# Optimization experiments

Hardware: AMD Instinct MI355X
Metric: run time of the kernel (lower is better)

Reference implementation:

```python
import jax, jax.numpy as jnp
import numpy as np

B, I, O, K = 4096, 1024, 1024, 16

def setup_inputs() -> dict:
    key = jax.random.key(0)
    k1, k2 = jax.random.split(key)
    x = jax.random.normal(k1, (B, I), dtype=jnp.float32)
    weights = jax.random.normal(k2, (O, I, K), dtype=jnp.float32)
    bias = jnp.zeros((O,), dtype=jnp.float32)
    centers = jnp.linspace(-1.0, 1.0, K, dtype=jnp.float32)
    widths = jnp.full((K,), 0.1, dtype=jnp.float32)
    return {"x": x, "weights": weights, "bias": bias, "centers": centers, "widths": widths}

def reference(x, weights, bias, centers, widths):
    # Gaussian RBF basis: [B, I, K]
    diff = x[:, :, None] - centers[None, None, :]
    kernels = jnp.exp(-(diff ** 2) / (2.0 * widths[None, None, :] ** 2))
    # Contraction over input_dim and num_kernels (GEMM-equivalent)
    out = jnp.einsum('bik,oik->bo', kernels, weights)
    return out + bias
```

## Files before the change

### kernel.cpp

```cpp
#include <hip/hip_runtime.h>
#include <hip/hip_bf16.h>


#define B_DIM 4096
#define I_DIM 1024
#define O_DIM 1024
#define NK 16
#define KD (I_DIM * NK)

typedef unsigned short u16;
typedef __attribute__((ext_vector_type(8))) __bf16 bf16x8;
typedef __attribute__((ext_vector_type(4))) float f32x4;
typedef __attribute__((ext_vector_type(8))) unsigned short u16x8;

typedef const __attribute__((address_space(1))) unsigned short gu16;
typedef __attribute__((address_space(3))) unsigned short lu16;

static __device__ __forceinline__ u16 f2bf(float f) {
  unsigned u = __float_as_uint(f);
  u += 0x7FFFu + ((u >> 16) & 1u);
  return (u16)(u >> 16);
}

__global__ void __launch_bounds__(256) rbf_feat(const float* __restrict__ x,
                                                u16* __restrict__ feat,
                                                const float* __restrict__ centers,
                                                const float* __restrict__ widths) {
  const int idx = blockIdx.x * 256 + threadIdx.x;
  const float xv = x[idx];
  u16x8 lo, hi;
#pragma unroll
  for (int k = 0; k < 16; ++k) {
    const float c = centers[k];
    const float w = widths[k];
    const float s = -0.5f * __builtin_amdgcn_rcpf(w * w);
    const float d = xv - c;
    const u16 h = f2bf(__expf(d * d * s));
    if (k < 8) lo[k] = h; else hi[k - 8] = h;
  }
  u16x8* dst = (u16x8*)(feat + (size_t)idx * 16);
  dst[0] = lo;
  dst[1] = hi;
}

__global__ void __launch_bounds__(256) cvt_w(const float4* __restrict__ w,
                                             u16x8* __restrict__ wb) {
  const size_t i = (size_t)blockIdx.x * 256 + threadIdx.x;
  const float4 a = w[2 * i];
  const float4 b = w[2 * i + 1];
  u16x8 o;
  o[0] = f2bf(a.x); o[1] = f2bf(a.y); o[2] = f2bf(a.z); o[3] = f2bf(a.w);
  o[4] = f2bf(b.x); o[5] = f2bf(b.y); o[6] = f2bf(b.z); o[7] = f2bf(b.w);
  wb[i] = o;
}

static __device__ __forceinline__ void stage_half(const u16* __restrict__ g,
                                                  u16* __restrict__ lds, int t) {
#pragma unroll
  for (int j = 0; j < 2; ++j) {
    const int chunk = j * 512 + t;
    const int row = chunk >> 3, slot = chunk & 7;
    const int c = slot ^ (row & 7);
    __builtin_amdgcn_global_load_lds((gu16*)(g + (size_t)row * KD + c * 8),
                                     (lu16*)(lds + chunk * 8), 16, 0, 0);
  }
}

#define NT 64

__global__ void __launch_bounds__(512, 2)
gemm8(const u16* __restrict__ A, const u16* __restrict__ Bm,
      float* __restrict__ part) {
  __shared__ u16 sA[2][2][128 * 64];
  __shared__ u16 sB[2][2][128 * 64];

  const int t = threadIdx.x;
  const int bm = blockIdx.x;
  const int bn = blockIdx.y;
  const int kz = blockIdx.z;
  const int wid = t >> 6, l = t & 63;
  const int wr = wid >> 2, wc = wid & 3;
  const int lm = l & 15, lk = l >> 4;

  const u16* aT = A + (size_t)(bm * 256) * KD + kz * 4096;
  const u16* bT = Bm + (size_t)(bn * 256) * KD + kz * 4096;

  const int swz0 = ((0 * 4 + lk) ^ (lm & 7)) * 8;
  const int swz1 = ((1 * 4 + lk) ^ (lm & 7)) * 8;
  const int arow = wr * 64 + lm;
  const int brow = wc * 32 + lm;

  f32x4 acc[8][4];
#pragma unroll
  for (int i = 0; i < 8; ++i)
#pragma unroll
    for (int j = 0; j < 4; ++j)
      acc[i][j] = (f32x4){0.f, 0.f, 0.f, 0.f};

  stage_half(aT, &sA[0][0][0], t);
  stage_half(aT + (size_t)128 * KD, &sA[0][1][0], t);
  stage_half(bT, &sB[0][0][0], t);
  stage_half(bT + (size_t)128 * KD, &sB[0][1][0], t);
  asm volatile("s_waitcnt vmcnt(0)" ::: "memory");
  __builtin_amdgcn_s_barrier();

  for (int T = 0; T < NT; ++T) {
    const int c = T & 1;

    if (T + 1 < NT) {
      const int kn = (T + 1) * 64;
      stage_half(aT + kn, &sA[c ^ 1][0][0], t);
      stage_half(aT + (size_t)128 * KD + kn, &sA[c ^ 1][1][0], t);
      stage_half(bT + kn, &sB[c ^ 1][0][0], t);
      stage_half(bT + (size_t)128 * KD + kn, &sB[c ^ 1][1][0], t);
    }

    bf16x8 aq[4][2], aq2[4][2], b0[2][2], b1[2][2];
#pragma unroll
    for (int mi = 0; mi < 4; ++mi) {
      aq[mi][0]  = *(const bf16x8*)&sA[c][0][(arow + mi * 16) * 64 + swz0];
      aq[mi][1]  = *(const bf16x8*)&sA[c][0][(arow + mi * 16) * 64 + swz1];
      aq2[mi][0] = *(const bf16x8*)&sA[c][1][(arow + mi * 16) * 64 + swz0];
      aq2[mi][1] = *(const bf16x8*)&sA[c][1][(arow + mi * 16) * 64 + swz1];
    }
#pragma unroll
    for (int ni = 0; ni < 2; ++ni) {
      b0[ni][0] = *(const bf16x8*)&sB[c][0][(brow + ni * 16) * 64 + swz0];
      b0[ni][1] = *(const bf16x8*)&sB[c][0][(brow + ni * 16) * 64 + swz1];
      b1[ni][0] = *(const bf16x8*)&sB[c][1][(brow + ni * 16) * 64 + swz0];
      b1[ni][1] = *(const bf16x8*)&sB[c][1][(brow + ni * 16) * 64 + swz1];
    }

    __builtin_amdgcn_s_setprio(1);
#pragma unroll
    for (int mi = 0; mi < 4; ++mi)
#pragma unroll
      for (int ni = 0; ni < 2; ++ni)
#pragma unroll
        for (int kk = 0; kk < 2; ++kk)
          acc[mi][ni] = __builtin_amdgcn_mfma_f32_16x16x32_bf16(
              aq[mi][kk], b0[ni][kk], acc[mi][ni], 0, 0, 0);
#pragma unroll
    for (int mi = 0; mi < 4; ++mi)
#pragma unroll
      for (int ni = 0; ni < 2; ++ni)
#pragma unroll
        for (int kk = 0; kk < 2; ++kk)
          acc[mi][2 + ni] = __builtin_amdgcn_mfma_f32_16x16x32_bf16(
              aq[mi][kk], b1[ni][kk], acc[mi][2 + ni], 0, 0, 0);
#pragma unroll
    for (int mi = 0; mi < 4; ++mi)
#pragma unroll
      for (int ni = 0; ni < 2; ++ni)
#pragma unroll
        for (int kk = 0; kk < 2; ++kk)
          acc[4 + mi][2 + ni] = __builtin_amdgcn_mfma_f32_16x16x32_bf16(
              aq2[mi][kk], b1[ni][kk], acc[4 + mi][2 + ni], 0, 0, 0);
#pragma unroll
    for (int mi = 0; mi < 4; ++mi)
#pragma unroll
      for (int ni = 0; ni < 2; ++ni)
#pragma unroll
        for (int kk = 0; kk < 2; ++kk)
          acc[4 + mi][ni] = __builtin_amdgcn_mfma_f32_16x16x32_bf16(
              aq2[mi][kk], b0[ni][kk], acc[4 + mi][ni], 0, 0, 0);
    __builtin_amdgcn_s_setprio(0);

    asm volatile("s_waitcnt vmcnt(0)" ::: "memory");
    __builtin_amdgcn_s_barrier();
  }

  float* pW = part + (size_t)kz * ((size_t)B_DIM * O_DIM);
#pragma unroll
  for (int qa = 0; qa < 2; ++qa)
#pragma unroll
    for (int mi = 0; mi < 4; ++mi)
#pragma unroll
      for (int qb = 0; qb < 2; ++qb)
#pragma unroll
        for (int ni = 0; ni < 2; ++ni) {
          const int row0 = bm * 256 + qa * 128 + wr * 64 + mi * 16 + lk * 4;
          const int col = bn * 256 + qb * 128 + wc * 32 + ni * 16 + lm;
#pragma unroll
          for (int j = 0; j < 4; ++j)
            pW[(size_t)(row0 + j) * O_DIM + col] = acc[qa * 4 + mi][qb * 2 + ni][j];
        }
}

__global__ void __launch_bounds__(256) reduce4(const float4* __restrict__ p,
                                               const float4* __restrict__ bias4,
                                               float4* __restrict__ out) {
  const int i = blockIdx.x * 256 + threadIdx.x;
  const size_t s = (size_t)B_DIM * O_DIM / 4;
  const float4 a = p[i], b = p[i + s], c = p[i + 2 * s], d = p[i + 3 * s];
  const float4 bb = bias4[i & 255];
  float4 r;
  r.x = a.x + b.x + c.x + d.x + bb.x;
  r.y = a.y + b.y + c.y + d.y + bb.y;
  r.z = a.z + b.z + c.z + d.z + bb.z;
  r.w = a.w + b.w + c.w + d.w + bb.w;
  out[i] = r;
}

#define BM 128
#define BN 64
#define BK 64

__global__ void __launch_bounds__(256, 2) gemm_bt(const u16* __restrict__ A,
                                                  const u16* __restrict__ Bm,
                                                  const float* __restrict__ bias,
                                                  float* __restrict__ C) {
  __shared__ u16 sA[BM * BK];
  __shared__ u16 sB[BN * BK];

  const int t = threadIdx.x;
  const int bm = blockIdx.x, bn = blockIdx.y;
  const int wid = t >> 6, l = t & 63;
  const int wr = wid >> 1, wc = wid & 1;
  const int lm = l & 15, lk = l >> 4;

  const u16* aG = A + (size_t)bm * BM * KD;
  const u16* bG = Bm + (size_t)bn * BN * KD;

  f32x4 acc[4][2];
#pragma unroll
  for (int mi = 0; mi < 4; ++mi)
#pragma unroll
    for (int ni = 0; ni < 2; ++ni)
      acc[mi][ni] = (f32x4){0.f, 0.f, 0.f, 0.f};

  for (int kt = 0; kt < KD; kt += BK) {
#pragma unroll
    for (int j = 0; j < 4; ++j) {
      const int chunk = j * 256 + t;
      const int row = chunk >> 3, slot = chunk & 7;
      const int c = slot ^ (row & 7);
      __builtin_amdgcn_global_load_lds((gu16*)(aG + (size_t)row * KD + kt + c * 8),
                                       (lu16*)(sA + chunk * 8), 16, 0, 0);
    }
#pragma unroll
    for (int j = 0; j < 2; ++j) {
      const int chunk = j * 256 + t;
      const int row = chunk >> 3, slot = chunk & 7;
      const int c = slot ^ (row & 7);
      __builtin_amdgcn_global_load_lds((gu16*)(bG + (size_t)row * KD + kt + c * 8),
                                       (lu16*)(sB + chunk * 8), 16, 0, 0);
    }
    __syncthreads();
#pragma unroll
    for (int kk = 0; kk < 2; ++kk) {
      const int s = (kk * 4 + lk) ^ (lm & 7);
      bf16x8 af[4], bfr[2];
#pragma unroll
      for (int mi = 0; mi < 4; ++mi)
        af[mi] = *(const bf16x8*)(sA + (wr * 64 + mi * 16 + lm) * BK + s * 8);
#pragma unroll
      for (int ni = 0; ni < 2; ++ni)
        bfr[ni] = *(const bf16x8*)(sB + (wc * 32 + ni * 16 + lm) * BK + s * 8);
#pragma unroll
      for (int mi = 0; mi < 4; ++mi)
#pragma unroll
        for (int ni = 0; ni < 2; ++ni)
          acc[mi][ni] = __builtin_amdgcn_mfma_f32_16x16x32_bf16(af[mi], bfr[ni],
                                                                acc[mi][ni], 0, 0, 0);
    }
    __syncthreads();
  }

#pragma unroll
  for (int ni = 0; ni < 2; ++ni) {
    const int col = bn * BN + wc * 32 + ni * 16 + lm;
    const float bv = bias[col];
#pragma unroll
    for (int mi = 0; mi < 4; ++mi) {
      const int row0 = bm * BM + wr * 64 + mi * 16 + lk * 4;
#pragma unroll
      for (int j = 0; j < 4; ++j)
        C[(size_t)(row0 + j) * O_DIM + col] = acc[mi][ni][j] + bv;
    }
  }
}

extern "C" void kernel_launch(void* const* d_in, const int* in_sizes, int n_in,
                              void* d_out, int out_size, void* d_ws, size_t ws_size,
                              hipStream_t stream) {
  const float* x = (const float*)d_in[0];
  const float* w = (const float*)d_in[1];
  const float* bias = (const float*)d_in[2];
  const float* centers = (const float*)d_in[3];
  const float* widths = (const float*)d_in[4];
  float* out = (float*)d_out;

  u16* feat = (u16*)d_ws;
  u16* wb = (u16*)((char*)d_ws + (size_t)B_DIM * KD * 2);
  float* part = (float*)((char*)d_ws + (size_t)B_DIM * KD * 2 + (size_t)O_DIM * KD * 2);

  rbf_feat<<<(B_DIM * I_DIM) / 256, 256, 0, stream>>>(x, feat, centers, widths);
  cvt_w<<<(O_DIM * KD) / (256 * 8), 256, 0, stream>>>((const float4*)w, (u16x8*)wb);

  const size_t need = (size_t)B_DIM * KD * 2 + (size_t)O_DIM * KD * 2 +
                      4ull * B_DIM * O_DIM * 4;
  if (ws_size >= need) {
    dim3 grid(B_DIM / 256, O_DIM / 256, 4);
    gemm8<<<grid, 512, 0, stream>>>(feat, wb, part);
    reduce4<<<(B_DIM * O_DIM / 4) / 256, 256, 0, stream>>>(
        (const float4*)part, (const float4*)bias, (float4*)out);
  } else {
    dim3 grid(B_DIM / BM, O_DIM / BN);
    gemm_bt<<<grid, 256, 0, stream>>>(feat, wb, bias, out);
  }
}
```

Before: 197.3 us.

## Prefetch first K-half tiles two stages ahead with triple-buffered LDS

Splits the A/B shared buffers into per-half arrays, triple-buffering the first 128-row halves and double-buffering the second halves. First halves are loaded two iterations ahead while second halves stay one ahead, and the end-of-iteration wait is relaxed to vmcnt(4) so the newest loads stay in flight across the barrier. This aims to hide more global-to-LDS latency behind MFMA work, at the cost of raising LDS use to the full 160KB and adding more complex indexing.

Result: no change. 198.6 us (+0.6%).

```diff
diff --git a/kernel.cpp b/kernel.cpp
--- a/kernel.cpp
+++ b/kernel.cpp
@@ -71,8 +71,10 @@
 __global__ void __launch_bounds__(512, 2)
 gemm8(const u16* __restrict__ A, const u16* __restrict__ Bm,
       float* __restrict__ part) {
-  __shared__ u16 sA[2][2][128 * 64];
-  __shared__ u16 sB[2][2][128 * 64];
+  __shared__ u16 sA0[3][128 * 64];
+  __shared__ u16 sB0[3][128 * 64];
+  __shared__ u16 sA1[2][128 * 64];
+  __shared__ u16 sB1[2][128 * 64];
 
   const int t = threadIdx.x;
   const int bm = blockIdx.x;
@@ -97,38 +99,44 @@
     for (int j = 0; j < 4; ++j)
       acc[i][j] = (f32x4){0.f, 0.f, 0.f, 0.f};
 
-  stage_half(aT, &sA[0][0][0], t);
-  stage_half(aT + (size_t)128 * KD, &sA[0][1][0], t);
-  stage_half(bT, &sB[0][0][0], t);
-  stage_half(bT + (size_t)128 * KD, &sB[0][1][0], t);
-  asm volatile("s_waitcnt vmcnt(0)" ::: "memory");
+  stage_half(aT, &sA0[0][0], t);
+  stage_half(aT + (size_t)128 * KD, &sA1[0][0], t);
+  stage_half(bT, &sB0[0][0], t);
+  stage_half(bT + (size_t)128 * KD, &sB1[0][0], t);
+  stage_half(bT + 64, &sB0[1][0], t);
+  stage_half(aT + 64, &sA0[1][0], t);
+  asm volatile("s_waitcnt vmcnt(4)" ::: "memory");
   __builtin_amdgcn_s_barrier();
 
   for (int T = 0; T < NT; ++T) {
-    const int c = T & 1;
+    const int c3 = T % 3;
+    const int c2 = T & 1;
 
     if (T + 1 < NT) {
-      const int kn = (T + 1) * 64;
-      stage_half(aT + kn, &sA[c ^ 1][0][0], t);
-      stage_half(aT + (size_t)128 * KD + kn, &sA[c ^ 1][1][0], t);
-      stage_half(bT + kn, &sB[c ^ 1][0][0], t);
-      stage_half(bT + (size_t)128 * KD + kn, &sB[c ^ 1][1][0], t);
+      const int kn1 = (T + 1) * 64;
+      stage_half(aT + (size_t)128 * KD + kn1, &sA1[(T + 1) & 1][0], t);
+      stage_half(bT + (size_t)128 * KD + kn1, &sB1[(T + 1) & 1][0], t);
+    }
+    if (T + 2 < NT) {
+      const int kn2 = (T + 2) * 64;
+      stage_half(bT + kn2, &sB0[(T + 2) % 3][0], t);
+      stage_half(aT + kn2, &sA0[(T + 2) % 3][0], t);
     }
 
     bf16x8 aq[4][2], aq2[4][2], b0[2][2], b1[2][2];
 #pragma unroll
     for (int mi = 0; mi < 4; ++mi) {
-      aq[mi][0]  = *(const bf16x8*)&sA[c][0][(arow + mi * 16) * 64 + swz0];
-      aq[mi][1]  = *(const bf16x8*)&sA[c][0][(arow + mi * 16) * 64 + swz1];
-      aq2[mi][0] = *(const bf16x8*)&sA[c][1][(arow + mi * 16) * 64 + swz0];
-      aq2[mi][1] = *(const bf16x8*)&sA[c][1][(arow + mi * 16) * 64 + swz1];
+      aq[mi][0]  = *(const bf16x8*)&sA0[c3][(arow + mi * 16) * 64 + swz0];
+      aq[mi][1]  = *(const bf16x8*)&sA0[c3][(arow + mi * 16) * 64 + swz1];
+      aq2[mi][0] = *(const bf16x8*)&sA1[c2][(arow + mi * 16) * 64 + swz0];
+      aq2[mi][1] = *(const bf16x8*)&sA1[c2][(arow + mi * 16) * 64 + swz1];
     }
 #pragma unroll
     for (int ni = 0; ni < 2; ++ni) {
-      b0[ni][0] = *(const bf16x8*)&sB[c][0][(brow + ni * 16) * 64 + swz0];
-      b0[ni][1] = *(const bf16x8*)&sB[c][0][(brow + ni * 16) * 64 + swz1];
-      b1[ni][0] = *(const bf16x8*)&sB[c][1][(brow + ni * 16) * 64 + swz0];
-      b1[ni][1] = *(const bf16x8*)&sB[c][1][(brow + ni * 16) * 64 + swz1];
+      b0[ni][0] = *(const bf16x8*)&sB0[c3][(brow + ni * 16) * 64 + swz0];
+      b0[ni][1] = *(const bf16x8*)&sB0[c3][(brow + ni * 16) * 64 + swz1];
+      b1[ni][0] = *(const bf16x8*)&sB1[c2][(brow + ni * 16) * 64 + swz0];
+      b1[ni][1] = *(const bf16x8*)&sB1[c2][(brow + ni * 16) * 64 + swz1];
     }
 
     __builtin_amdgcn_s_setprio(1);
@@ -166,7 +174,8 @@
               aq2[mi][kk], b0[ni][kk], acc[4 + mi][ni], 0, 0, 0);
     __builtin_amdgcn_s_setprio(0);
 
-    asm volatile("s_waitcnt vmcnt(0)" ::: "memory");
+    if (T + 2 < NT) asm volatile("s_waitcnt vmcnt(4)" ::: "memory");
+    else            asm volatile("s_waitcnt vmcnt(0)" ::: "memory");
     __builtin_amdgcn_s_barrier();
   }
 
```

## Shrink split-K GEMM tile to 128x128 with 256 threads and remapped block order

Applied to the files above, without the earlier changes.

Replaces the 256x256 tile, 512-thread split-K GEMM with a 128x128 tile, 256-thread kernel. Each wave keeps a 64x64 output subtile, and blocks are launched four times as many (1024 total). Block IDs are remapped so consecutive blocks spread across XCD-like groups of 8 and share A/B panels in cache. The aim is better load balance and occupancy across CUs. In exchange, the smaller tiles reuse operands less and generate more global/LDS traffic per FLOP.

Result: slower. 286.7 us (+45.3%).

```diff
diff --git a/kernel.cpp b/kernel.cpp
--- a/kernel.cpp
+++ b/kernel.cpp
@@ -54,11 +54,11 @@
   wb[i] = o;
 }
 
-static __device__ __forceinline__ void stage_half(const u16* __restrict__ g,
+static __device__ __forceinline__ void stage_tile(const u16* __restrict__ g,
                                                   u16* __restrict__ lds, int t) {
 #pragma unroll
-  for (int j = 0; j < 2; ++j) {
-    const int chunk = j * 512 + t;
+  for (int j = 0; j < 4; ++j) {
+    const int chunk = j * 256 + t;
     const int row = chunk >> 3, slot = chunk & 7;
     const int c = slot ^ (row & 7);
     __builtin_amdgcn_global_load_lds((gu16*)(g + (size_t)row * KD + c * 8),
@@ -68,39 +68,39 @@
 
 #define NT 64
 
-__global__ void __launch_bounds__(512, 2)
-gemm8(const u16* __restrict__ A, const u16* __restrict__ Bm,
-      float* __restrict__ part) {
-  __shared__ u16 sA[2][2][128 * 64];
-  __shared__ u16 sB[2][2][128 * 64];
+__global__ void __launch_bounds__(256, 2)
+gemm128(const u16* __restrict__ A, const u16* __restrict__ Bm,
+        float* __restrict__ part) {
+  __shared__ u16 sA[2][128 * 64];
+  __shared__ u16 sB[2][128 * 64];
 
   const int t = threadIdx.x;
-  const int bm = blockIdx.x;
-  const int bn = blockIdx.y;
-  const int kz = blockIdx.z;
+  const int lin = blockIdx.x + 32 * (blockIdx.y + 8 * blockIdx.z);
+  const int work = (lin & 7) * 128 + (lin >> 3);
+  const int bm = work & 31;
+  const int bn = (work >> 5) & 7;
+  const int kz = work >> 8;
   const int wid = t >> 6, l = t & 63;
-  const int wr = wid >> 2, wc = wid & 3;
+  const int wr = wid >> 1, wc = wid & 1;
   const int lm = l & 15, lk = l >> 4;
 
-  const u16* aT = A + (size_t)(bm * 256) * KD + kz * 4096;
-  const u16* bT = Bm + (size_t)(bn * 256) * KD + kz * 4096;
+  const u16* aT = A + (size_t)(bm * 128) * KD + kz * 4096;
+  const u16* bT = Bm + (size_t)(bn * 128) * KD + kz * 4096;
 
   const int swz0 = ((0 * 4 + lk) ^ (lm & 7)) * 8;
   const int swz1 = ((1 * 4 + lk) ^ (lm & 7)) * 8;
   const int arow = wr * 64 + lm;
-  const int brow = wc * 32 + lm;
-
-  f32x4 acc[8][4];
-#pragma unroll
-  for (int i = 0; i < 8; ++i)
+  const int brow = wc * 64 + lm;
+
+  f32x4 acc[4][4];
+#pragma unroll
+  for (int i = 0; i < 4; ++i)
 #pragma unroll
     for (int j = 0; j < 4; ++j)
       acc[i][j] = (f32x4){0.f, 0.f, 0.f, 0.f};
 
-  stage_half(aT, &sA[0][0][0], t);
-  stage_half(aT + (size_t)128 * KD, &sA[0][1][0], t);
-  stage_half(bT, &sB[0][0][0], t);
-  stage_half(bT + (size_t)128 * KD, &sB[0][1][0], t);
+  stage_tile(aT, &sA[0][0], t);
+  stage_tile(bT, &sB[0][0], t);
   asm volatile("s_waitcnt vmcnt(0)" ::: "memory");
   __builtin_amdgcn_s_barrier();
 
@@ -108,62 +108,31 @@
     const int c = T & 1;
 
     if (T + 1 < NT) {
-      const int kn = (T + 1) * 64;
-      stage_half(aT + kn, &sA[c ^ 1][0][0], t);
-      stage_half(aT + (size_t)128 * KD + kn, &sA[c ^ 1][1][0], t);
-      stage_half(bT + kn, &sB[c ^ 1][0][0], t);
-      stage_half(bT + (size_t)128 * KD + kn, &sB[c ^ 1][1][0], t);
-    }
-
-    bf16x8 aq[4][2], aq2[4][2], b0[2][2], b1[2][2];
+      stage_tile(aT + (T + 1) * 64, &sA[c ^ 1][0], t);
+      stage_tile(bT + (T + 1) * 64, &sB[c ^ 1][0], t);
+    }
+
+    bf16x8 aq[4][2], bq[4][2];
 #pragma unroll
     for (int mi = 0; mi < 4; ++mi) {
-      aq[mi][0]  = *(const bf16x8*)&sA[c][0][(arow + mi * 16) * 64 + swz0];
-      aq[mi][1]  = *(const bf16x8*)&sA[c][0][(arow + mi * 16) * 64 + swz1];
-      aq2[mi][0] = *(const bf16x8*)&sA[c][1][(arow + mi * 16) * 64 + swz0];
-      aq2[mi][1] = *(const bf16x8*)&sA[c][1][(arow + mi * 16) * 64 + swz1];
-    }
-#pragma unroll
-    for (int ni = 0; ni < 2; ++ni) {
-      b0[ni][0] = *(const bf16x8*)&sB[c][0][(brow + ni * 16) * 64 + swz0];
-      b0[ni][1] = *(const bf16x8*)&sB[c][0][(brow + ni * 16) * 64 + swz1];
-      b1[ni][0] = *(const bf16x8*)&sB[c][1][(brow + ni * 16) * 64 + swz0];
-      b1[ni][1] = *(const bf16x8*)&sB[c][1][(brow + ni * 16) * 64 + swz1];
+      aq[mi][0] = *(const bf16x8*)&sA[c][(arow + mi * 16) * 64 + swz0];
+      aq[mi][1] = *(const bf16x8*)&sA[c][(arow + mi * 16) * 64 + swz1];
+    }
+#pragma unroll
+    for (int ni = 0; ni < 4; ++ni) {
+      bq[ni][0] = *(const bf16x8*)&sB[c][(brow + ni * 16) * 64 + swz0];
+      bq[ni][1] = *(const bf16x8*)&sB[c][(brow + ni * 16) * 64 + swz1];
     }
 
     __builtin_amdgcn_s_setprio(1);
 #pragma unroll
     for (int mi = 0; mi < 4; ++mi)
 #pragma unroll
-      for (int ni = 0; ni < 2; ++ni)
+      for (int ni = 0; ni < 4; ++ni)
 #pragma unroll
         for (int kk = 0; kk < 2; ++kk)
           acc[mi][ni] = __builtin_amdgcn_mfma_f32_16x16x32_bf16(
-              aq[mi][kk], b0[ni][kk], acc[mi][ni], 0, 0, 0);
-#pragma unroll
-    for (int mi = 0; mi < 4; ++mi)
-#pragma unroll
-      for (int ni = 0; ni < 2; ++ni)
-#pragma unroll
-        for (int kk = 0; kk < 2; ++kk)
-          acc[mi][2 + ni] = __builtin_amdgcn_mfma_f32_16x16x32_bf16(
-              aq[mi][kk], b1[ni][kk], acc[mi][2 + ni], 0, 0, 0);
-#pragma unroll
-    for (int mi = 0; mi < 4; ++mi)
-#pragma unroll
-      for (int ni = 0; ni < 2; ++ni)
-#pragma unroll
-        for (int kk = 0; kk < 2; ++kk)
-          acc[4 + mi][2 + ni] = __builtin_amdgcn_mfma_f32_16x16x32_bf16(
-              aq2[mi][kk], b1[ni][kk], acc[4 + mi][2 + ni], 0, 0, 0);
-#pragma unroll
-    for (int mi = 0; mi < 4; ++mi)
-#pragma unroll
-      for (int ni = 0; ni < 2; ++ni)
-#pragma unroll
-        for (int kk = 0; kk < 2; ++kk)
-          acc[4 + mi][ni] = __builtin_amdgcn_mfma_f32_16x16x32_bf16(
-              aq2[mi][kk], b0[ni][kk], acc[4 + mi][ni], 0, 0, 0);
+              aq[mi][kk], bq[ni][kk], acc[mi][ni], 0, 0, 0);
     __builtin_amdgcn_s_setprio(0);
 
     asm volatile("s_waitcnt vmcnt(0)" ::: "memory");
@@ -172,19 +141,16 @@
 
   float* pW = part + (size_t)kz * ((size_t)B_DIM * O_DIM);
 #pragma unroll
-  for (int qa = 0; qa < 2; ++qa)
-#pragma unroll
-    for (int mi = 0; mi < 4; ++mi)
-#pragma unroll
-      for (int qb = 0; qb < 2; ++qb)
-#pragma unroll
-        for (int ni = 0; ni < 2; ++ni) {
-          const int row0 = bm * 256 + qa * 128 + wr * 64 + mi * 16 + lk * 4;
-          const int col = bn * 256 + qb * 128 + wc * 32 + ni * 16 + lm;
-#pragma unroll
-          for (int j = 0; j < 4; ++j)
-            pW[(size_t)(row0 + j) * O_DIM + col] = acc[qa * 4 + mi][qb * 2 + ni][j];
-        }
+  for (int mi = 0; mi < 4; ++mi) {
+    const int row0 = bm * 128 + wr * 64 + mi * 16 + lk * 4;
+#pragma unroll
+    for (int ni = 0; ni < 4; ++ni) {
+      const int col = bn * 128 + wc * 64 + ni * 16 + lm;
+#pragma unroll
+      for (int j = 0; j < 4; ++j)
+        pW[(size_t)(row0 + j) * O_DIM + col] = acc[mi][ni][j];
+    }
+  }
 }
 
 __global__ void __launch_bounds__(256) reduce4(const float4* __restrict__ p,
@@ -301,8 +267,8 @@
   const size_t need = (size_t)B_DIM * KD * 2 + (size_t)O_DIM * KD * 2 +
                       4ull * B_DIM * O_DIM * 4;
   if (ws_size >= need) {
-    dim3 grid(B_DIM / 256, O_DIM / 256, 4);
-    gemm8<<<grid, 512, 0, stream>>>(feat, wb, part);
+    dim3 grid(B_DIM / 128, O_DIM / 128, 4);
+    gemm128<<<grid, 256, 0, stream>>>(feat, wb, part);
     reduce4<<<(B_DIM * O_DIM / 4) / 256, 256, 0, stream>>>(
         (const float4*)part, (const float4*)bias, (float4*)out);
   } else {
```
